# Optimization experiments

Hardware: AMD Instinct MI355X
Metric: run time of the kernel (lower is better)

The kernel has to match this reference:

```python
import jax, jax.numpy as jnp
import numpy as np
import math

E = 2048         # n_embd
H = 16           # num query head pairs (num_heads)
HKV = 8          # num_kv_heads
NREP = H // HKV  # 2
HD = E // H // 2 # head_dim = 64
DEPTH = 12
LAMBDA_INIT = 0.8 - 0.6 * math.exp(-0.3 * DEPTH)
EPS = 1e-6


def setup_inputs() -> dict:
    key = jax.random.key(0)
    ks = jax.random.split(key, 10)
    s = lambda fan_in: 1.0 / np.sqrt(fan_in)
    return {
        "x": jax.random.normal(ks[0], (2, 2048, E), jnp.float32),
        "Wq": jax.random.normal(ks[1], (E, E), jnp.float32) * s(E),
        "Wk": jax.random.normal(ks[2], (E, E // NREP), jnp.float32) * s(E),
        "Wv": jax.random.normal(ks[3], (E, E // NREP), jnp.float32) * s(E),
        "Wo": jax.random.normal(ks[4], (E, E), jnp.float32) * s(E),
        "lam_q1": jax.random.normal(ks[5], (HD,), jnp.float32) * 0.1,
        "lam_k1": jax.random.normal(ks[6], (HD,), jnp.float32) * 0.1,
        "lam_q2": jax.random.normal(ks[7], (HD,), jnp.float32) * 0.1,
        "lam_k2": jax.random.normal(ks[8], (HD,), jnp.float32) * 0.1,
        "g": jnp.ones((2 * HD,), jnp.float32),  # RMSNorm weight
    }


def _rotary(x, cos, sin):
    # x: [B, T, nh, HD]; cos/sin: [T, HD//2]
    d = x.shape[-1] // 2
    x1, x2 = x[..., :d], x[..., d:]
    c = cos[None, :, None, :]
    si = sin[None, :, None, :]
    return jnp.concatenate([x1 * c + x2 * si, -x1 * si + x2 * c], axis=-1)


def reference(x, Wq, Wk, Wv, Wo, lam_q1, lam_k1, lam_q2, lam_k2, g):
    B, T, _ = x.shape
    q = (x @ Wq).reshape(B, T, 2 * H, HD)
    k = (x @ Wk).reshape(B, T, 2 * HKV, HD)
    v = (x @ Wv).reshape(B, T, HKV, 2 * HD)

    inv_freq = 1.0 / (10000.0 ** (jnp.arange(0, HD, 2, dtype=jnp.float32) / HD))
    freqs = jnp.arange(T, dtype=jnp.float32)[:, None] * inv_freq[None, :]
    cos, sin = jnp.cos(freqs), jnp.sin(freqs)
    q = _rotary(q, cos, sin)
    k = _rotary(k, cos, sin)

    q = jnp.transpose(q, (0, 2, 1, 3)) * (HD ** -0.5)   # [B, 2H, T, HD]
    k = jnp.repeat(jnp.transpose(k, (0, 2, 1, 3)), NREP, axis=1)  # [B, 2H, T, HD]
    v = jnp.repeat(jnp.transpose(v, (0, 2, 1, 3)), NREP, axis=1)  # [B, H, T, 2HD]

    scores = jnp.einsum('bhtd,bhsd->bhts', q, k)
    scores = jnp.nan_to_num(scores)
    mask = jnp.triu(jnp.full((T, T), -jnp.inf, scores.dtype), 1)
    scores = scores + mask
    p = jax.nn.softmax(scores.astype(jnp.float32), axis=-1).astype(scores.dtype)

    lam1 = jnp.exp(jnp.sum(lam_q1 * lam_k1))
    lam2 = jnp.exp(jnp.sum(lam_q2 * lam_k2))
    lam = lam1 - lam2 + LAMBDA_INIT

    p = p.reshape(B, H, 2, T, T)
    diff = p[:, :, 0] - lam * p[:, :, 1]               # [B, H, T, T]
    attn = jnp.einsum('bhts,bhsd->bhtd', diff, v)      # [B, H, T, 2HD]

    # RMSNorm over last dim (2*HD)
    attn = attn * jax.lax.rsqrt(jnp.mean(attn * attn, axis=-1, keepdims=True) + EPS) * g
    attn = attn * (1.0 - LAMBDA_INIT)
    attn = jnp.transpose(attn, (0, 2, 1, 3)).reshape(B, T, E)
    return attn @ Wo
```

## Files before the change

kernel.cpp:

```cpp
#include <hip/hip_runtime.h>

#define T_SEQ 2048

typedef __bf16 bf16x8 __attribute__((ext_vector_type(8)));
typedef float f32x4 __attribute__((ext_vector_type(4)));
typedef unsigned short u16;

__device__ __forceinline__ u16 f2b(float f) {
  unsigned u = __float_as_uint(f);
  unsigned r = 0x7fffu + ((u >> 16) & 1u);
  return (u16)((u + r) >> 16);
}
__device__ __forceinline__ float b2f(u16 v) {
  return __uint_as_float(((unsigned)v) << 16);
}
__device__ __forceinline__ f32x4 mfma16(bf16x8 a, bf16x8 b, f32x4 c) {
  return __builtin_amdgcn_mfma_f32_16x16x32_bf16(a, b, c, 0, 0, 0);
}
__device__ __forceinline__ unsigned pkhi(float lo, float hi) {
  return __builtin_amdgcn_perm(__float_as_uint(hi), __float_as_uint(lo), 0x07060302u);
}
#if defined(__has_builtin)
#if __has_builtin(__builtin_amdgcn_exp2f)
#define HAVE_RAW_EXP2 1
#endif
#endif
__device__ __forceinline__ float exp2r(float x) {
#ifdef HAVE_RAW_EXP2
  return __builtin_amdgcn_exp2f(x);
#else
  float r;
  asm("v_exp_f32 %0, %1" : "=v"(r) : "v"(x));
  return r;
#endif
}
__device__ __forceinline__ void glds16(const void* g, void* s) {
  __builtin_amdgcn_global_load_lds(
      (const __attribute__((address_space(1))) void*)(uintptr_t)g,
      (__attribute__((address_space(3))) void*)(unsigned)(uintptr_t)s, 16, 0, 0);
}

__global__ void lam_kernel(const float* __restrict__ q1, const float* __restrict__ k1,
                           const float* __restrict__ q2, const float* __restrict__ k2,
                           float* __restrict__ outp) {
  int l = threadIdx.x;
  float a = q1[l] * k1[l];
  float c = q2[l] * k2[l];
  #pragma unroll
  for (int off = 32; off > 0; off >>= 1) {
    a += __shfl_down(a, off);
    c += __shfl_down(c, off);
  }
  if (l == 0) outp[0] = expf(a) - expf(c) + 0.7836057665316244f;
}

__global__ __launch_bounds__(256) void convert_kernel(const float* __restrict__ in,
                                                      u16* __restrict__ outp, int n) {
  int i = (blockIdx.x * 256 + threadIdx.x) * 4;
  if (i >= n) return;
  float4 v = *(const float4*)(in + i);
  ushort4 pk;
  pk.x = f2b(v.x); pk.y = f2b(v.y); pk.z = f2b(v.z); pk.w = f2b(v.w);
  *(ushort4*)(outp + i) = pk;
}

__global__ __launch_bounds__(256) void transposeW_kernel(const float* __restrict__ Wq,
                                                         const float* __restrict__ Wk,
                                                         const float* __restrict__ Wv,
                                                         const float* __restrict__ Wo,
                                                         u16* __restrict__ outp) {
  __shared__ float tile[32][33];
  const int ro0 = blockIdx.y * 32;
  const int r0 = blockIdx.x * 32;
  const float* src; int C, cbase;
  if (ro0 < 2048)      { src = Wq; C = 2048; cbase = 0; }
  else if (ro0 < 3072) { src = Wk; C = 1024; cbase = 2048; }
  else if (ro0 < 4096) { src = Wv; C = 1024; cbase = 3072; }
  else                 { src = Wo; C = 2048; cbase = 4096; }
  const int cs0 = ro0 - cbase;
  const int tx = threadIdx.x & 31, ty = threadIdx.x >> 5;
  #pragma unroll
  for (int k2 = 0; k2 < 4; k2++)
    tile[ty * 4 + k2][tx] = src[(size_t)(r0 + ty * 4 + k2) * C + cs0 + tx];
  __syncthreads();
  #pragma unroll
  for (int k2 = 0; k2 < 4; k2++)
    outp[(size_t)(ro0 + ty * 4 + k2) * 2048 + r0 + tx] = f2b(tile[tx][ty * 4 + k2]);
}

template <bool OUT_BF16>
__global__ __launch_bounds__(256) void gemm128_kernel(const u16* __restrict__ A,
                                                      const u16* __restrict__ BT,
                                                      void* __restrict__ C, int N, int K) {
  __shared__ alignas(16) u16 As[128 * 64];
  __shared__ alignas(16) u16 Bs[128 * 64];
  const int tid = threadIdx.x, w = tid >> 6, lane = tid & 63;
  const int l15 = lane & 15, quad = lane >> 4;
  const int m0 = blockIdx.y * 128, n0 = blockIdx.x * 128;
  const int wm = (w >> 1) * 64, wn = (w & 1) * 64;
  const int lr = lane >> 3, slot = lane & 7, csw = slot ^ lr;
  f32x4 acc[4][4];
  #pragma unroll
  for (int mt = 0; mt < 4; mt++)
    #pragma unroll
    for (int nt = 0; nt < 4; nt++) acc[mt][nt] = (f32x4){0.f, 0.f, 0.f, 0.f};
  const u16* Ag = A + (size_t)(m0 + w * 32 + lr) * K + csw * 8;
  const u16* Bg = BT + (size_t)(n0 + w * 32 + lr) * K + csw * 8;
  u16* Asd = As + (w * 32) * 64;
  u16* Bsd = Bs + (w * 32) * 64;
  for (int kt = 0; kt < K; kt += 64) {
    #pragma unroll
    for (int i = 0; i < 4; i++) {
      glds16(Ag + kt + (size_t)(i * 8) * K, Asd + i * 512);
      glds16(Bg + kt + (size_t)(i * 8) * K, Bsd + i * 512);
    }
    __syncthreads();
    #pragma unroll
    for (int kk = 0; kk < 2; kk++) {
      bf16x8 am[4], bn[4];
      #pragma unroll
      for (int t = 0; t < 4; t++) {
        const int ra = wm + t * 16 + l15;
        am[t] = *(const bf16x8*)&As[ra * 64 + (((kk * 4 + quad) ^ (ra & 7)) << 3)];
        const int rb = wn + t * 16 + l15;
        bn[t] = *(const bf16x8*)&Bs[rb * 64 + (((kk * 4 + quad) ^ (rb & 7)) << 3)];
      }
      #pragma unroll
      for (int mt = 0; mt < 4; mt++)
        #pragma unroll
        for (int nt = 0; nt < 4; nt++) acc[mt][nt] = mfma16(am[mt], bn[nt], acc[mt][nt]);
    }
    __syncthreads();
  }
  const int row = m0 + wm + quad * 4;
  #pragma unroll
  for (int mt = 0; mt < 4; mt++) {
    #pragma unroll
    for (int nt = 0; nt < 4; nt++) {
      const int col = n0 + wn + nt * 16 + l15;
      #pragma unroll
      for (int rr = 0; rr < 4; rr++) {
        if (OUT_BF16)
          ((u16*)C)[(size_t)(row + mt * 16 + rr) * N + col] = f2b(acc[mt][nt][rr]);
        else
          ((float*)C)[(size_t)(row + mt * 16 + rr) * N + col] = acc[mt][nt][rr];
      }
    }
  }
}

#define STAGE_HALF(TILE, ROLE, BUF)                                                     \
  do {                                                                                  \
    const u16* sp_ = ((ROLE) == 0 || (ROLE) == 3 ? Ag : Bg) +                           \
                     (size_t)((ROLE) >= 2 ? 128 : 0) * K + (size_t)(TILE) * 64;         \
    u16* dp_ = ((ROLE) == 0 || (ROLE) == 3 ? &As[BUF][0] : &Bs[BUF][0]) +               \
               (((ROLE) >= 2 ? 128 : 0) + w * 8) * 64;                                  \
    glds16(sp_, dp_);                                                                   \
    glds16(sp_ + (size_t)64 * K, dp_ + 4096);                                           \
  } while (0)

#define PHASE(I, J, BUF, NEWA, NEWB, BN, STILE, SROLE, SBUF, DOVM)                      \
  do {                                                                                  \
    if (NEWA) {                                                                         \
      _Pragma("unroll") for (int u_ = 0; u_ < 4; u_++) {                                \
        const int ar_ = ((I) * 4 + u_) * 32 + wm * 16 + l15;                            \
        _Pragma("unroll") for (int kk_ = 0; kk_ < 2; kk_++)                             \
            am[u_][kk_] = *(const bf16x8*)&As[BUF][ar_ * 64 +                           \
                              (((kk_ * 4 + quad) ^ (ar_ & 7)) << 3)];                   \
      }                                                                                 \
    }                                                                                   \
    if (NEWB) {                                                                         \
      _Pragma("unroll") for (int v_ = 0; v_ < 2; v_++) {                                \
        const int br_ = ((J) * 2 + v_) * 64 + wn * 16 + l15;                            \
        _Pragma("unroll") for (int kk_ = 0; kk_ < 2; kk_++)                             \
            BN[v_][kk_] = *(const bf16x8*)&Bs[BUF][br_ * 64 +                           \
                              (((kk_ * 4 + quad) ^ (br_ & 7)) << 3)];                   \
      }                                                                                 \
    }                                                                                   \
    STAGE_HALF(STILE, SROLE, SBUF);                                                     \
    __builtin_amdgcn_s_barrier();                                                       \
    asm volatile("s_waitcnt lgkmcnt(0)" ::: "memory");                                  \
    __builtin_amdgcn_sched_barrier(0);                                                  \
    __builtin_amdgcn_s_setprio(1);                                                      \
    _Pragma("unroll") for (int u_ = 0; u_ < 4; u_++)                                    \
        _Pragma("unroll") for (int v_ = 0; v_ < 2; v_++) {                              \
      acc[(I) * 4 + u_][(J) * 2 + v_] =                                                 \
          mfma16(am[u_][0], BN[v_][0], acc[(I) * 4 + u_][(J) * 2 + v_]);                \
      acc[(I) * 4 + u_][(J) * 2 + v_] =                                                 \
          mfma16(am[u_][1], BN[v_][1], acc[(I) * 4 + u_][(J) * 2 + v_]);                \
    }                                                                                   \
    __builtin_amdgcn_s_setprio(0);                                                      \
    if (DOVM) asm volatile("s_waitcnt vmcnt(6)" ::: "memory");                          \
    __builtin_amdgcn_s_barrier();                                                       \
  } while (0)

__global__ __launch_bounds__(512, 2) void gemm256_kernel(const u16* __restrict__ A,
                                                         const u16* __restrict__ BT,
                                                         u16* __restrict__ C, int N, int K) {
  __shared__ alignas(16) u16 As[2][256 * 64];
  __shared__ alignas(16) u16 Bs[2][256 * 64];
  const int tid = threadIdx.x, w = tid >> 6, lane = tid & 63;
  const int l15 = lane & 15, quad = lane >> 4;
  const int wm = w >> 2, wn = w & 3;
  const int lr = lane >> 3, slot = lane & 7, csw = slot ^ lr;
  const int m0 = blockIdx.y * 256, n0 = blockIdx.x * 256;
  const int nkt = K >> 6;

  f32x4 acc[8][4];
  #pragma unroll
  for (int r = 0; r < 8; r++)
    #pragma unroll
    for (int s = 0; s < 4; s++) acc[r][s] = (f32x4){0.f, 0.f, 0.f, 0.f};

  const u16* Ag = A + (size_t)(m0 + w * 8 + lr) * K + csw * 8;
  const u16* Bg = BT + (size_t)(n0 + w * 8 + lr) * K + csw * 8;

  bf16x8 am[4][2], bn0[2][2], bn1[2][2];

  STAGE_HALF(0, 0, 0); STAGE_HALF(0, 1, 0); STAGE_HALF(0, 2, 0); STAGE_HALF(0, 3, 0);
  STAGE_HALF(1, 0, 1); STAGE_HALF(1, 1, 1); STAGE_HALF(1, 2, 1);
  asm volatile("s_waitcnt vmcnt(6)" ::: "memory");
  __builtin_amdgcn_s_barrier();

  #pragma unroll 1
  for (int t = 0; t < nkt; t += 2) {
    PHASE(0, 0, 0, 1, 1, bn0, t + 1, 3, 1, 0);
    PHASE(0, 1, 0, 0, 1, bn1, t + 2, 0, 0, 0);
    PHASE(1, 0, 0, 1, 0, bn0, t + 2, 1, 0, 0);
    PHASE(1, 1, 0, 0, 0, bn1, t + 2, 2, 0, 1);
    PHASE(0, 0, 1, 1, 1, bn0, t + 2, 3, 0, 0);
    PHASE(0, 1, 1, 0, 1, bn1, t + 3, 0, 1, 0);
    PHASE(1, 0, 1, 1, 0, bn0, t + 3, 1, 1, 0);
    PHASE(1, 1, 1, 0, 0, bn1, t + 3, 2, 1, 1);
  }

  const int crow = m0 + wm * 16 + quad * 4;
  const int ccol = n0 + wn * 16 + l15;
  #pragma unroll
  for (int r = 0; r < 8; r++)
    #pragma unroll
    for (int s = 0; s < 4; s++)
      #pragma unroll
      for (int rr = 0; rr < 4; rr++)
        C[(size_t)(crow + r * 32 + rr) * N + ccol + s * 64] = f2b(acc[r][s][rr]);
}

__global__ __launch_bounds__(256) void rotary_kernel(const u16* __restrict__ qkv,
                                                     u16* __restrict__ Qb,
                                                     u16* __restrict__ Kb, float qscale) {
  int idx = blockIdx.x * 256 + threadIdx.x;
  int i = idx & 31;
  int bt = (idx >> 5) & 4095;
  int hh = idx >> 17;
  int t = bt & (T_SEQ - 1), b = bt >> 11;
  bool isq = hh < 32;
  int col = isq ? hh * 64 : 2048 + (hh - 32) * 64;
  size_t inb = (size_t)bt * 4096 + col + i;
  float x1 = b2f(qkv[inb]);
  float x2 = b2f(qkv[inb + 32]);
  float invf = exp2f(-(float)i * 0.4152410118609203f);
  float ang = (float)t * invf;
  float c = cosf(ang), s = sinf(ang);
  float scale = isq ? qscale : 1.0f;
  float o1 = (x1 * c + x2 * s) * scale;
  float o2 = (x2 * c - x1 * s) * scale;
  u16* outp = isq ? (Qb + (size_t)(b * 32 + hh) * (T_SEQ * 64))
                  : (Kb + (size_t)(b * 16 + hh - 32) * (T_SEQ * 64));
  size_t ob = (size_t)t * 64 + i;
  outp[ob] = f2b(o1);
  outp[ob + 32] = f2b(o2);
}

__global__ __launch_bounds__(256) void vtrans_kernel(const u16* __restrict__ qkv,
                                                     u16* __restrict__ outp) {
  __shared__ unsigned tile[32][33];
  int bh = blockIdx.z;
  int t0 = blockIdx.x * 32, dv0 = blockIdx.y * 32;
  int tx = threadIdx.x & 31, ty = threadIdx.x >> 5;
  int bt_base = (bh >> 3) * T_SEQ;
  int col = 3072 + (bh & 7) * 128 + dv0 + tx;
  #pragma unroll
  for (int k2 = 0; k2 < 4; k2++)
    tile[ty * 4 + k2][tx] = qkv[(size_t)(bt_base + t0 + ty * 4 + k2) * 4096 + col];
  __syncthreads();
  const int stile = t0 >> 6;
  const int sold = (t0 & 63) + tx;
  const int slo = sold & 31, hb = sold >> 5;
  const int sp = hb * 32 + ((slo >> 2) & 3) * 8 + ((slo >> 4) & 1) * 4 + (slo & 3);
  #pragma unroll
  for (int k2 = 0; k2 < 4; k2++) {
    int dv = dv0 + ty * 4 + k2;
    outp[(((size_t)bh * 32 + stile) * 128 + dv) * 64 + sp] = (u16)tile[tx][ty * 4 + k2];
  }
}

__global__ __launch_bounds__(256) void attn_kernel(const u16* __restrict__ Qb,
                                                   const u16* __restrict__ Kb,
                                                   const u16* __restrict__ Vt,
                                                   const float* __restrict__ lamp,
                                                   const float* __restrict__ g,
                                                   u16* __restrict__ attn_out) {
  __shared__ alignas(16) u16 Ks[2][64 * 64];
  __shared__ alignas(16) u16 Vs[2][128 * 64];
  __shared__ alignas(16) u16 Ps[4][16][136];
  const int pr = blockIdx.x;
  const int bh = blockIdx.y;
  const int b = bh >> 4, h = bh & 15;
  const int tid = threadIdx.x, w = tid >> 6, lane = tid & 63;
  const int l15 = lane & 15, quad = lane >> 4;
  const int lr = lane >> 3, slot = lane & 7, csw = slot ^ lr;
  const float lam = lamp[0];

  const u16* Kg = Kb + (size_t)(b * 16 + h) * (T_SEQ * 64) + (w * 16 + lr) * 64 + csw * 8;
  const u16* Vg = Vt + (size_t)(b * 8 + (h >> 1)) * (T_SEQ * 128) + w * 2048 + lr * 64 + csw * 8;
  u16* kd[2] = {&Ks[0][w * 1024], &Ks[1][w * 1024]};
  u16* vd[2] = {&Vs[0][w * 2048], &Vs[1][w * 2048]};

  #pragma unroll 1
  for (int half = 0; half < 2; half++) {
    const int tt = half ? 31 - pr : pr;
    const int qb = tt * 64 + w * 16;
    const int qglob = qb + l15;

    bf16x8 qf[2][2];
    #pragma unroll
    for (int e = 0; e < 2; e++)
      #pragma unroll
      for (int kk = 0; kk < 2; kk++)
        qf[e][kk] = *(const bf16x8*)&Qb[((size_t)(b * 32 + 2 * h + e) * T_SEQ + qb + l15) * 64 +
                                        kk * 32 + quad * 8];

    f32x4 o[2][8];
    float lsum[2] = {0.f, 0.f};
    #pragma unroll
    for (int e = 0; e < 2; e++)
      #pragma unroll
      for (int nt = 0; nt < 8; nt++) o[e][nt] = (f32x4){0.f, 0.f, 0.f, 0.f};

    {
      glds16(Kg, kd[0]); glds16(Kg + 512, kd[0] + 512);
      glds16(Vg, vd[0]); glds16(Vg + 512, vd[0] + 512);
      glds16(Vg + 1024, vd[0] + 1024); glds16(Vg + 1536, vd[0] + 1536);
    }
    __syncthreads();

    #pragma unroll 1
    for (int st = 0; st <= tt; st++) {
      const int buf = st & 1;
      if (st < tt) {
        const u16* kp = Kg + (size_t)(st + 1) * 4096;
        const u16* vp = Vg + (size_t)(st + 1) * 8192;
        glds16(kp, kd[buf ^ 1]); glds16(kp + 512, kd[buf ^ 1] + 512);
        glds16(vp, vd[buf ^ 1]); glds16(vp + 512, vd[buf ^ 1] + 512);
        glds16(vp + 1024, vd[buf ^ 1] + 1024); glds16(vp + 1536, vd[buf ^ 1] + 1536);
      }

      bf16x8 kf[4][2];
      #pragma unroll
      for (int j = 0; j < 4; j++) {
        const int rk = j * 16 + l15;
        #pragma unroll
        for (int kk = 0; kk < 2; kk++)
          kf[j][kk] = *(const bf16x8*)&Ks[buf][rk * 64 + (((kk * 4 + quad) ^ (rk & 7)) << 3)];
      }

      bf16x8 pa[2][2];
      #pragma unroll
      for (int e = 0; e < 2; e++) {
        f32x4 sc[4];
        __builtin_amdgcn_s_setprio(1);
        #pragma unroll
        for (int j = 0; j < 4; j++) {
          f32x4 z = {0.f, 0.f, 0.f, 0.f};
          z = mfma16(kf[j][0], qf[e][0], z);
          sc[j] = mfma16(kf[j][1], qf[e][1], z);
        }
        __builtin_amdgcn_s_setprio(0);
        if (st == tt) {
          #pragma unroll
          for (int j = 0; j < 4; j++) {
            int srow = st * 64 + j * 16 + quad * 4;
            #pragma unroll
            for (int rr = 0; rr < 4; rr++)
              if (srow + rr > qglob) sc[j][rr] = -1e30f;
          }
        }
        float ls = 0.f;
        union { unsigned u[8]; bf16x8 v[2]; } pk;
        #pragma unroll
        for (int j = 0; j < 4; j++) {
          #pragma unroll
          for (int rr = 0; rr < 4; rr++) {
            float p = exp2r(sc[j][rr]);
            sc[j][rr] = p;
            ls += p;
          }
          pk.u[j * 2] = pkhi(sc[j][0], sc[j][1]);
          pk.u[j * 2 + 1] = pkhi(sc[j][2], sc[j][3]);
        }
        pa[e][0] = pk.v[0];
        pa[e][1] = pk.v[1];
        lsum[e] += ls;
      }
      __builtin_amdgcn_s_setprio(1);
      #pragma unroll
      for (int nt = 0; nt < 8; nt++) {
        const int rv = nt * 16 + l15;
        bf16x8 vf0 = *(const bf16x8*)&Vs[buf][rv * 64 + ((quad ^ (rv & 7)) << 3)];
        bf16x8 vf1 = *(const bf16x8*)&Vs[buf][rv * 64 + (((4 + quad) ^ (rv & 7)) << 3)];
        o[0][nt] = mfma16(vf0, pa[0][0], o[0][nt]);
        o[0][nt] = mfma16(vf1, pa[0][1], o[0][nt]);
        o[1][nt] = mfma16(vf0, pa[1][0], o[1][nt]);
        o[1][nt] = mfma16(vf1, pa[1][1], o[1][nt]);
      }
      __builtin_amdgcn_s_setprio(0);
      __syncthreads();
    }

    float l0 = lsum[0], l1 = lsum[1];
    l0 += __shfl_xor(l0, 16); l0 += __shfl_xor(l0, 32);
    l1 += __shfl_xor(l1, 16); l1 += __shfl_xor(l1, 32);
    const float il0 = 1.f / l0, il1 = lam / l1;
    float ssq = 0.f;
    #pragma unroll
    for (int nt = 0; nt < 8; nt++)
      #pragma unroll
      for (int rr = 0; rr < 4; rr++) {
        float v = o[0][nt][rr] * il0 - o[1][nt][rr] * il1;
        o[0][nt][rr] = v;
        ssq += v * v;
      }
    ssq += __shfl_xor(ssq, 16);
    ssq += __shfl_xor(ssq, 32);
    const float rsc = rsqrtf(ssq * (1.f / 128.f) + 1e-6f) * 0.2163942334683756f;
    #pragma unroll
    for (int nt = 0; nt < 8; nt++) {
      float4 gv = *(const float4*)&g[nt * 16 + quad * 4];
      uint2 pk;
      pk.x = (unsigned)f2b(o[0][nt][0] * rsc * gv.x) |
             ((unsigned)f2b(o[0][nt][1] * rsc * gv.y) << 16);
      pk.y = (unsigned)f2b(o[0][nt][2] * rsc * gv.z) |
             ((unsigned)f2b(o[0][nt][3] * rsc * gv.w) << 16);
      *(uint2*)&Ps[w][l15][nt * 16 + quad * 4] = pk;
    }
    asm volatile("s_waitcnt lgkmcnt(0)" ::: "memory");
    __builtin_amdgcn_sched_barrier(0);
    #pragma unroll
    for (int i = 0; i < 4; i++) {
      const int r = (lane >> 4) + i * 4, c = (lane & 15) * 8;
      bf16x8 ov = *(const bf16x8*)&Ps[w][r][c];
      *(bf16x8*)&attn_out[(size_t)(b * T_SEQ + qb + r) * 2048 + h * 128 + c] = ov;
    }
    __syncthreads();
  }
}

extern "C" void kernel_launch(void* const* d_in, const int* in_sizes, int n_in, void* d_out,
                              int out_size, void* d_ws, size_t ws_size, hipStream_t stream) {
  const float* x = (const float*)d_in[0];
  const float* Wq = (const float*)d_in[1];
  const float* Wk = (const float*)d_in[2];
  const float* Wv = (const float*)d_in[3];
  const float* Wo = (const float*)d_in[4];
  const float* lq1 = (const float*)d_in[5];
  const float* lk1 = (const float*)d_in[6];
  const float* lq2 = (const float*)d_in[7];
  const float* lk2 = (const float*)d_in[8];
  const float* g = (const float*)d_in[9];

  char* ws = (char*)d_ws;
  u16* WT = (u16*)(ws);
  u16* xbf = (u16*)(ws + 25165824);
  u16* QKV = (u16*)(ws + 41943040);
  u16* Qb = (u16*)(ws + 75497472);
  u16* Kb = (u16*)(ws + 92274688);
  u16* Vt = (u16*)(ws + 100663296);
  u16* Attn = (u16*)(ws + 109051904);
  float* lam = (float*)(ws + 125829120);

  lam_kernel<<<1, 64, 0, stream>>>(lq1, lk1, lq2, lk2, lam);
  convert_kernel<<<8192, 256, 0, stream>>>(x, xbf, 8388608);
  transposeW_kernel<<<dim3(64, 192), 256, 0, stream>>>(Wq, Wk, Wv, Wo, WT);
  gemm256_kernel<<<dim3(16, 16), 512, 0, stream>>>(xbf, WT, QKV, 4096, 2048);
  rotary_kernel<<<24576, 256, 0, stream>>>(QKV, Qb, Kb, 0.18033688011112042f);
  vtrans_kernel<<<dim3(64, 4, 16), 256, 0, stream>>>(QKV, Vt);
  attn_kernel<<<dim3(16, 32), 256, 0, stream>>>(Qb, Kb, Vt, lam, g, Attn);
  gemm128_kernel<false><<<dim3(16, 32), 256, 0, stream>>>(Attn, WT + (size_t)4096 * 2048, d_out,
                                                          2048, 2048);
}
```

Baseline: 320.1 us.

## Launch one attention block per query tile, heaviest tiles first, alias LDS

Drops the paired causal-balancing loop where each block handled query tiles pr and 31-pr. It now launches 32x32 blocks, each covering one query tile, ordered heaviest first (tt = 31 - blockIdx.x). The output staging buffer now aliases the K/V shared memory, cutting LDS per block from about 66KB to 48KB so more blocks can be resident per CU. The trade-off is a larger grid whose per-block work varies, relying on the hardware scheduler to balance it instead of the static pairing.

```diff
diff --git a/kernel.cpp b/kernel.cpp
--- a/kernel.cpp
+++ b/kernel.cpp
@@ -300,10 +300,11 @@
                                                    const float* __restrict__ lamp,
                                                    const float* __restrict__ g,
                                                    u16* __restrict__ attn_out) {
-  __shared__ alignas(16) u16 Ks[2][64 * 64];
-  __shared__ alignas(16) u16 Vs[2][128 * 64];
-  __shared__ alignas(16) u16 Ps[4][16][136];
-  const int pr = blockIdx.x;
+  __shared__ alignas(16) char smem[49152];
+  u16* const Ks0 = (u16*)smem;
+  u16* const Vs0 = (u16*)(smem + 16384);
+  u16* const Psb = (u16*)smem;
+  const int tt = 31 - blockIdx.x;
   const int bh = blockIdx.y;
   const int b = bh >> 4, h = bh & 15;
   const int tid = threadIdx.x, w = tid >> 6, lane = tid & 63;
@@ -313,145 +314,142 @@
 
   const u16* Kg = Kb + (size_t)(b * 16 + h) * (T_SEQ * 64) + (w * 16 + lr) * 64 + csw * 8;
   const u16* Vg = Vt + (size_t)(b * 8 + (h >> 1)) * (T_SEQ * 128) + w * 2048 + lr * 64 + csw * 8;
-  u16* kd[2] = {&Ks[0][w * 1024], &Ks[1][w * 1024]};
-  u16* vd[2] = {&Vs[0][w * 2048], &Vs[1][w * 2048]};
+  u16* kd[2] = {Ks0 + w * 1024, Ks0 + 4096 + w * 1024};
+  u16* vd[2] = {Vs0 + w * 2048, Vs0 + 8192 + w * 2048};
+
+  const int qb = tt * 64 + w * 16;
+  const int qglob = qb + l15;
+
+  bf16x8 qf[2][2];
+  #pragma unroll
+  for (int e = 0; e < 2; e++)
+    #pragma unroll
+    for (int kk = 0; kk < 2; kk++)
+      qf[e][kk] = *(const bf16x8*)&Qb[((size_t)(b * 32 + 2 * h + e) * T_SEQ + qb + l15) * 64 +
+                                      kk * 32 + quad * 8];
+
+  f32x4 o[2][8];
+  float lsum[2] = {0.f, 0.f};
+  #pragma unroll
+  for (int e = 0; e < 2; e++)
+    #pragma unroll
+    for (int nt = 0; nt < 8; nt++) o[e][nt] = (f32x4){0.f, 0.f, 0.f, 0.f};
+
+  {
+    glds16(Kg, kd[0]); glds16(Kg + 512, kd[0] + 512);
+    glds16(Vg, vd[0]); glds16(Vg + 512, vd[0] + 512);
+    glds16(Vg + 1024, vd[0] + 1024); glds16(Vg + 1536, vd[0] + 1536);
+  }
+  __syncthreads();
 
   #pragma unroll 1
-  for (int half = 0; half < 2; half++) {
-    const int tt = half ? 31 - pr : pr;
-    const int qb = tt * 64 + w * 16;
-    const int qglob = qb + l15;
-
-    bf16x8 qf[2][2];
-    #pragma unroll
-    for (int e = 0; e < 2; e++)
+  for (int st = 0; st <= tt; st++) {
+    const int buf = st & 1;
+    const u16* Ksb = Ks0 + buf * 4096;
+    const u16* Vsb = Vs0 + buf * 8192;
+    if (st < tt) {
+      const u16* kp = Kg + (size_t)(st + 1) * 4096;
+      const u16* vp = Vg + (size_t)(st + 1) * 8192;
+      glds16(kp, kd[buf ^ 1]); glds16(kp + 512, kd[buf ^ 1] + 512);
+      glds16(vp, vd[buf ^ 1]); glds16(vp + 512, vd[buf ^ 1] + 512);
+      glds16(vp + 1024, vd[buf ^ 1] + 1024); glds16(vp + 1536, vd[buf ^ 1] + 1536);
+    }
+
+    bf16x8 kf[4][2];
+    #pragma unroll
+    for (int j = 0; j < 4; j++) {
+      const int rk = j * 16 + l15;
       #pragma unroll
       for (int kk = 0; kk < 2; kk++)
-        qf[e][kk] = *(const bf16x8*)&Qb[((size_t)(b * 32 + 2 * h + e) * T_SEQ + qb + l15) * 64 +
-                                        kk * 32 + quad * 8];
-
-    f32x4 o[2][8];
-    float lsum[2] = {0.f, 0.f};
-    #pragma unroll
-    for (int e = 0; e < 2; e++)
-      #pragma unroll
-      for (int nt = 0; nt < 8; nt++) o[e][nt] = (f32x4){0.f, 0.f, 0.f, 0.f};
-
-    {
-      glds16(Kg, kd[0]); glds16(Kg + 512, kd[0] + 512);
-      glds16(Vg, vd[0]); glds16(Vg + 512, vd[0] + 512);
-      glds16(Vg + 1024, vd[0] + 1024); glds16(Vg + 1536, vd[0] + 1536);
-    }
-    __syncthreads();
-
-    #pragma unroll 1
-    for (int st = 0; st <= tt; st++) {
-      const int buf = st & 1;
-      if (st < tt) {
-        const u16* kp = Kg + (size_t)(st + 1) * 4096;
-        const u16* vp = Vg + (size_t)(st + 1) * 8192;
-        glds16(kp, kd[buf ^ 1]); glds16(kp + 512, kd[buf ^ 1] + 512);
-        glds16(vp, vd[buf ^ 1]); glds16(vp + 512, vd[buf ^ 1] + 512);
-        glds16(vp + 1024, vd[buf ^ 1] + 1024); glds16(vp + 1536, vd[buf ^ 1] + 1536);
+        kf[j][kk] = *(const bf16x8*)&Ksb[rk * 64 + (((kk * 4 + quad) ^ (rk & 7)) << 3)];
+    }
+
+    bf16x8 pa[2][2];
+    #pragma unroll
+    for (int e = 0; e < 2; e++) {
+      f32x4 sc[4];
+      __builtin_amdgcn_s_setprio(1);
+      #pragma unroll
+      for (int j = 0; j < 4; j++) {
+        f32x4 z = {0.f, 0.f, 0.f, 0.f};
+        z = mfma16(kf[j][0], qf[e][0], z);
+        sc[j] = mfma16(kf[j][1], qf[e][1], z);
       }
-
-      bf16x8 kf[4][2];
-      #pragma unroll
-      for (int j = 0; j < 4; j++) {
-        const int rk = j * 16 + l15;
-        #pragma unroll
-        for (int kk = 0; kk < 2; kk++)
-          kf[j][kk] = *(const bf16x8*)&Ks[buf][rk * 64 + (((kk * 4 + quad) ^ (rk & 7)) << 3)];
-      }
-
-      bf16x8 pa[2][2];
-      #pragma unroll
-      for (int e = 0; e < 2; e++) {
-        f32x4 sc[4];
-        __builtin_amdgcn_s_setprio(1);
+      __builtin_amdgcn_s_setprio(0);
+      if (st == tt) {
         #pragma unroll
         for (int j = 0; j < 4; j++) {
-          f32x4 z = {0.f, 0.f, 0.f, 0.f};
-          z = mfma16(kf[j][0], qf[e][0], z);
-          sc[j] = mfma16(kf[j][1], qf[e][1], z);
+          int srow = st * 64 + j * 16 + quad * 4;
+          #pragma unroll
+          for (int rr = 0; rr < 4; rr++)
+            if (srow + rr > qglob) sc[j][rr] = -1e30f;
         }
-        __builtin_amdgcn_s_setprio(0);
-        if (st == tt) {
-          #pragma unroll
-          for (int j = 0; j < 4; j++) {
-            int srow = st * 64 + j * 16 + quad * 4;
-            #pragma unroll
-            for (int rr = 0; rr < 4; rr++)
-              if (srow + rr > qglob) sc[j][rr] = -1e30f;
-          }
+      }
+      float ls = 0.f;
+      union { unsigned u[8]; bf16x8 v[2]; } pk;
+      #pragma unroll
+      for (int j = 0; j < 4; j++) {
+        #pragma unroll
+        for (int rr = 0; rr < 4; rr++) {
+          float p = exp2r(sc[j][rr]);
+          sc[j][rr] = p;
+          ls += p;
         }
-        float ls = 0.f;
-        union { unsigned u[8]; bf16x8 v[2]; } pk;
-        #pragma unroll
-        for (int j = 0; j < 4; j++) {
-          #pragma unroll
-          for (int rr = 0; rr < 4; rr++) {
-            float p = exp2r(sc[j][rr]);
-            sc[j][rr] = p;
-            ls += p;
-          }
-          pk.u[j * 2] = pkhi(sc[j][0], sc[j][1]);
-          pk.u[j * 2 + 1] = pkhi(sc[j][2], sc[j][3]);
-        }
-        pa[e][0] = pk.v[0];
-        pa[e][1] = pk.v[1];
-        lsum[e] += ls;
+        pk.u[j * 2] = pkhi(sc[j][0], sc[j][1]);
+        pk.u[j * 2 + 1] = pkhi(sc[j][2], sc[j][3]);
       }
-      __builtin_amdgcn_s_setprio(1);
-      #pragma unroll
-      for (int nt = 0; nt < 8; nt++) {
-        const int rv = nt * 16 + l15;
-        bf16x8 vf0 = *(const bf16x8*)&Vs[buf][rv * 64 + ((quad ^ (rv & 7)) << 3)];
-        bf16x8 vf1 = *(const bf16x8*)&Vs[buf][rv * 64 + (((4 + quad) ^ (rv & 7)) << 3)];
-        o[0][nt] = mfma16(vf0, pa[0][0], o[0][nt]);
-        o[0][nt] = mfma16(vf1, pa[0][1], o[0][nt]);
-        o[1][nt] = mfma16(vf0, pa[1][0], o[1][nt]);
-        o[1][nt] = mfma16(vf1, pa[1][1], o[1][nt]);
-      }
-      __builtin_amdgcn_s_setprio(0);
-      __syncthreads();
-    }
-
-    float l0 = lsum[0], l1 = lsum[1];
-    l0 += __shfl_xor(l0, 16); l0 += __shfl_xor(l0, 32);
-    l1 += __shfl_xor(l1, 16); l1 += __shfl_xor(l1, 32);
-    const float il0 = 1.f / l0, il1 = lam / l1;
-    float ssq = 0.f;
-    #pragma unroll
-    for (int nt = 0; nt < 8; nt++)
-      #pragma unroll
-      for (int rr = 0; rr < 4; rr++) {
-        float v = o[0][nt][rr] * il0 - o[1][nt][rr] * il1;
-        o[0][nt][rr] = v;
-        ssq += v * v;
-      }
-    ssq += __shfl_xor(ssq, 16);
-    ssq += __shfl_xor(ssq, 32);
-    const float rsc = rsqrtf(ssq * (1.f / 128.f) + 1e-6f) * 0.2163942334683756f;
+      pa[e][0] = pk.v[0];
+      pa[e][1] = pk.v[1];
+      lsum[e] += ls;
+    }
+    __builtin_amdgcn_s_setprio(1);
     #pragma unroll
     for (int nt = 0; nt < 8; nt++) {
-      float4 gv = *(const float4*)&g[nt * 16 + quad * 4];
-      uint2 pk;
-      pk.x = (unsigned)f2b(o[0][nt][0] * rsc * gv.x) |
-             ((unsigned)f2b(o[0][nt][1] * rsc * gv.y) << 16);
-      pk.y = (unsigned)f2b(o[0][nt][2] * rsc * gv.z) |
-             ((unsigned)f2b(o[0][nt][3] * rsc * gv.w) << 16);
-      *(uint2*)&Ps[w][l15][nt * 16 + quad * 4] = pk;
-    }
-    asm volatile("s_waitcnt lgkmcnt(0)" ::: "memory");
-    __builtin_amdgcn_sched_barrier(0);
-    #pragma unroll
-    for (int i = 0; i < 4; i++) {
-      const int r = (lane >> 4) + i * 4, c = (lane & 15) * 8;
-      bf16x8 ov = *(const bf16x8*)&Ps[w][r][c];
-      *(bf16x8*)&attn_out[(size_t)(b * T_SEQ + qb + r) * 2048 + h * 128 + c] = ov;
-    }
+      const int rv = nt * 16 + l15;
+      bf16x8 vf0 = *(const bf16x8*)&Vsb[rv * 64 + ((quad ^ (rv & 7)) << 3)];
+      bf16x8 vf1 = *(const bf16x8*)&Vsb[rv * 64 + (((4 + quad) ^ (rv & 7)) << 3)];
+      o[0][nt] = mfma16(vf0, pa[0][0], o[0][nt]);
+      o[0][nt] = mfma16(vf1, pa[0][1], o[0][nt]);
+      o[1][nt] = mfma16(vf0, pa[1][0], o[1][nt]);
+      o[1][nt] = mfma16(vf1, pa[1][1], o[1][nt]);
+    }
+    __builtin_amdgcn_s_setprio(0);
     __syncthreads();
+  }
+
+  float l0 = lsum[0], l1 = lsum[1];
+  l0 += __shfl_xor(l0, 16); l0 += __shfl_xor(l0, 32);
+  l1 += __shfl_xor(l1, 16); l1 += __shfl_xor(l1, 32);
+  const float il0 = 1.f / l0, il1 = lam / l1;
+  float ssq = 0.f;
+  #pragma unroll
+  for (int nt = 0; nt < 8; nt++)
+    #pragma unroll
+    for (int rr = 0; rr < 4; rr++) {
+      float v = o[0][nt][rr] * il0 - o[1][nt][rr] * il1;
+      o[0][nt][rr] = v;
+      ssq += v * v;
+    }
+  ssq += __shfl_xor(ssq, 16);
+  ssq += __shfl_xor(ssq, 32);
+  const float rsc = rsqrtf(ssq * (1.f / 128.f) + 1e-6f) * 0.2163942334683756f;
+  #pragma unroll
+  for (int nt = 0; nt < 8; nt++) {
+    float4 gv = *(const float4*)&g[nt * 16 + quad * 4];
+    uint2 pk;
+    pk.x = (unsigned)f2b(o[0][nt][0] * rsc * gv.x) |
+           ((unsigned)f2b(o[0][nt][1] * rsc * gv.y) << 16);
+    pk.y = (unsigned)f2b(o[0][nt][2] * rsc * gv.z) |
+           ((unsigned)f2b(o[0][nt][3] * rsc * gv.w) << 16);
+    *(uint2*)&Psb[(w * 16 + l15) * 136 + nt * 16 + quad * 4] = pk;
+  }
+  asm volatile("s_waitcnt lgkmcnt(0)" ::: "memory");
+  __builtin_amdgcn_sched_barrier(0);
+  #pragma unroll
+  for (int i = 0; i < 4; i++) {
+    const int r = (lane >> 4) + i * 4, c = (lane & 15) * 8;
+    bf16x8 ov = *(const bf16x8*)&Psb[(w * 16 + r) * 136 + c];
+    *(bf16x8*)&attn_out[(size_t)(b * T_SEQ + qb + r) * 2048 + h * 128 + c] = ov;
   }
 }
 
@@ -484,7 +482,7 @@
   gemm256_kernel<<<dim3(16, 16), 512, 0, stream>>>(xbf, WT, QKV, 4096, 2048);
   rotary_kernel<<<24576, 256, 0, stream>>>(QKV, Qb, Kb, 0.18033688011112042f);
   vtrans_kernel<<<dim3(64, 4, 16), 256, 0, stream>>>(QKV, Vt);
-  attn_kernel<<<dim3(16, 32), 256, 0, stream>>>(Qb, Kb, Vt, lam, g, Attn);
+  attn_kernel<<<dim3(32, 32), 256, 0, stream>>>(Qb, Kb, Vt, lam, g, Attn);
   gemm128_kernel<false><<<dim3(16, 32), 256, 0, stream>>>(Attn, WT + (size_t)4096 * 2048, d_out,
                                                           2048, 2048);
 }
```

Result: slower. 361.3 us (+12.8%).
